# Kernel tuning notes

Measured on AMD Instinct MI355X. Metric: run time of the kernel, lower is better.

## Reference

```python
import jax, jax.numpy as jnp
import numpy as np

B, S, D, H, T = 64, 512, 1024, 1024, 9


def setup_inputs() -> dict:
    key = jax.random.key(0)
    ks = jax.random.split(key, 8)
    return {
        "input_": jax.random.normal(ks[0], (B, S, D), dtype=jnp.float32),
        "labels": jax.random.randint(ks[1], (B, S), 0, T),
        "attention_mask": jnp.ones((B, S), dtype=jnp.int32),
        # linear_1: input_dim -> hidden_dim (stored [in, out])
        "W1": (jax.random.normal(ks[2], (D, H), dtype=jnp.float32) * 0.02),
        "b1": jnp.zeros((H,), dtype=jnp.float32),
        # linear_2: hidden_dim -> tag_dim
        "W2": (jax.random.normal(ks[3], (H, T), dtype=jnp.float32) * 0.02),
        "b2": jnp.zeros((T,), dtype=jnp.float32),
        # torchcrf params: uniform(-0.1, 0.1)
        "start_trans": jax.random.uniform(ks[4], (T,), minval=-0.1, maxval=0.1),
        "end_trans": jax.random.uniform(ks[5], (T,), minval=-0.1, maxval=0.1),
        "trans": jax.random.uniform(ks[6], (T, T), minval=-0.1, maxval=0.1),
    }


def _crf_mean_llh(logits, tags, mask, start, end, trans):
    """torchcrf.CRF log-likelihood, reduction='mean'. logits [B,S,T]."""
    nb = logits.shape[0]
    em = jnp.transpose(logits, (1, 0, 2))          # [S,B,T] time-major
    tg = tags.T                                    # [S,B]
    m = mask.T.astype(logits.dtype)                # [S,B]
    bidx = jnp.arange(nb)

    # --- numerator: score of the gold path ---
    score0 = start[tg[0]] + em[0, bidx, tg[0]]

    def num_step(carry, x):
        score, last = carry
        em_t, tag_t, m_t = x
        score = score + (trans[last, tag_t] + em_t[bidx, tag_t]) * m_t
        last = jnp.where(m_t > 0, tag_t, last)
        return (score, last), None

    (score, last), _ = jax.lax.scan(num_step, (score0, tg[0]), (em[1:], tg[1:], m[1:]))
    score = score + end[last]

    # --- denominator: log-partition via logsumexp forward recurrence ---
    alpha0 = start[None, :] + em[0]                # [B,T]

    def part_step(alpha, x):
        em_t, m_t = x
        # [B, prev T, next T] semiring (log-sum-exp) matrix product
        nxt = jax.nn.logsumexp(alpha[:, :, None] + trans[None, :, :] + em_t[:, None, :], axis=1)
        alpha = jnp.where(m_t[:, None] > 0, nxt, alpha)
        return alpha, None

    alpha, _ = jax.lax.scan(part_step, alpha0, (em[1:], m[1:]))
    log_z = jax.nn.logsumexp(alpha + end[None, :], axis=1)

    return jnp.mean(score - log_z)


def reference(input_, labels, attention_mask, W1, b1, W2, b2, start_trans, end_trans, trans):
    # dropout layers are identity in eval mode
    h = input_ @ W1 + b1                           # [B,S,H]
    logits = h @ W2 + b2                           # [B,S,T]
    llh = _crf_mean_llh(logits, labels, attention_mask, start_trans, end_trans, trans)
    loss = -llh                                    # forward returns (-1*crf_llh, logits)
    return (loss, logits)
```

## Files before the change

kernel.cpp:

```cpp
#include <hip/hip_runtime.h>

#define BD 64
#define SD 512
#define DD 1024
#define HD 1024
#define TD 9
#define NSEG 16
#define SEGL 32
#define NEGI -1e30f

__device__ __forceinline__ float lse9(const float v[9]) {
    float m0 = fmaxf(v[0], v[1]);
    float m1 = fmaxf(v[2], v[3]);
    float m2 = fmaxf(v[4], v[5]);
    float m3 = fmaxf(v[6], v[7]);
    float mx = fmaxf(fmaxf(m0, m1), fmaxf(fmaxf(m2, m3), v[8]));
    float s = __expf(v[0] - mx) + __expf(v[1] - mx) + __expf(v[2] - mx)
            + __expf(v[3] - mx) + __expf(v[4] - mx) + __expf(v[5] - mx)
            + __expf(v[6] - mx) + __expf(v[7] - mx) + __expf(v[8] - mx);
    return mx + __logf(s);
}

__global__ __launch_bounds__(256) void k_w12(const float* __restrict__ W1,
                                             const float* __restrict__ b1,
                                             const float* __restrict__ W2,
                                             const float* __restrict__ b2,
                                             float* __restrict__ W12t,
                                             float* __restrict__ W12d,
                                             float* __restrict__ b12,
                                             float* __restrict__ out) {
    __shared__ float wred[4][TD];
    const int tid = threadIdx.x;
    const int wave = tid >> 6, lane = tid & 63;
    const int d = blockIdx.x;

    if (d == 0 && tid == 0) out[0] = 0.f;

    const float* row = (d < DD) ? (W1 + (size_t)d * HD) : b1;
    float4 x = ((const float4*)row)[tid];

    float w[36];
    const float4* wp = (const float4*)(W2 + (size_t)tid * 36);
#pragma unroll
    for (int u = 0; u < 9; u++) ((float4*)w)[u] = wp[u];

    float acc[TD];
#pragma unroll
    for (int t = 0; t < TD; t++)
        acc[t] = x.x * w[t] + x.y * w[9 + t] + x.z * w[18 + t] + x.w * w[27 + t];

#pragma unroll
    for (int t = 0; t < TD; t++) {
        float v = acc[t];
#pragma unroll
        for (int m = 1; m < 64; m <<= 1) v += __shfl_xor(v, m);
        acc[t] = v;
    }
    if (lane == 0) {
#pragma unroll
        for (int t = 0; t < TD; t++) wred[wave][t] = acc[t];
    }
    __syncthreads();
    if (tid < TD) {
        float s = wred[0][tid] + wred[1][tid] + wred[2][tid] + wred[3][tid];
        if (d < DD) {
            W12t[tid * DD + d] = s;
            W12d[d * TD + tid] = s;
        } else {
            b12[tid] = s + b2[tid];
        }
    }
}

__global__ __launch_bounds__(256) void k_gemm_seg(const float* __restrict__ X,
                                                  const float* __restrict__ W12t,
                                                  const float* __restrict__ b12,
                                                  const int* __restrict__ maskp,
                                                  const float* __restrict__ transp,
                                                  float* __restrict__ logits,
                                                  float* __restrict__ segP) {
    __shared__ float bufA[16 * 81];
    __shared__ float bufB[8 * 81];
    __shared__ float em[SEGL * TD];
    __shared__ int   mk[SEGL];
    __shared__ float tr[81];
    __shared__ float bb[TD];

    const int blk = blockIdx.x;
    const int b = blk >> 4, s = blk & 15;
    const int tid = threadIdx.x;
    const int wave = tid >> 6, lane = tid & 63;
    const int g = lane >> 4, l16 = lane & 15;
    const int grp = wave * 4 + g;
    const int t0 = s * SEGL;

    if (tid < TD) bb[tid] = b12[tid];
    if (tid < 81) tr[tid] = transp[tid];
    if (tid < SEGL) {
        int t = t0 + 1 + tid;
        mk[tid] = (t < SD) ? maskp[b * SD + t] : 0;
    }

    const int rowa = t0 + 1 + grp * 2;
    const int rowb_real = rowa + 1;
    const int rowb = (rowb_real < SD) ? rowb_real : (SD - 1);

    const float4* xr0 = (const float4*)(X + ((size_t)b * SD + rowa) * DD);
    const float4* xr1 = (const float4*)(X + ((size_t)b * SD + rowb) * DD);

    const float4* wr[TD];
#pragma unroll
    for (int t = 0; t < TD; t++)
        wr[t] = (const float4*)(W12t + (size_t)t * DD) + l16;

    float acc0[TD], acc1[TD];
#pragma unroll
    for (int t = 0; t < TD; t++) { acc0[t] = 0.f; acc1[t] = 0.f; }

#pragma unroll 4
    for (int k = 0; k < 16; k++) {
        float4 x0 = xr0[l16 + k * 16];
        float4 x1 = xr1[l16 + k * 16];
#pragma unroll
        for (int t = 0; t < TD; t++) {
            const float4 w = wr[t][k * 16];
            acc0[t] += x0.x * w.x + x0.y * w.y + x0.z * w.z + x0.w * w.w;
            acc1[t] += x1.x * w.x + x1.y * w.y + x1.z * w.z + x1.w * w.w;
        }
    }

#pragma unroll
    for (int t = 0; t < TD; t++) {
        float v0 = acc0[t], v1 = acc1[t];
        v0 += __shfl_xor(v0, 1); v1 += __shfl_xor(v1, 1);
        v0 += __shfl_xor(v0, 2); v1 += __shfl_xor(v1, 2);
        v0 += __shfl_xor(v0, 4); v1 += __shfl_xor(v1, 4);
        v0 += __shfl_xor(v0, 8); v1 += __shfl_xor(v1, 8);
        acc0[t] = v0; acc1[t] = v1;
    }

    if (l16 < TD) {
        float v0 = acc0[l16] + bb[l16];
        float v1 = acc1[l16] + bb[l16];
        em[(grp * 2) * TD + l16] = v0;
        em[(grp * 2 + 1) * TD + l16] = v1;
        float* o = logits + ((size_t)b * SD + rowa) * TD;
        o[l16] = v0;
        if (rowb_real < SD) o[TD + l16] = v1;
    }
    __syncthreads();

    for (int e = tid; e < 16 * 81; e += 256) {
        int p = e / 81, r = e - p * 81;
        int i = r / 9, j = r - i * 9;
        int la = 2 * p, lb = 2 * p + 1;
        int mA = mk[la], mB = mk[lb];
        float o;
        if (mA && mB) {
            float v[9];
#pragma unroll
            for (int k = 0; k < 9; k++)
                v[k] = tr[i * 9 + k] + em[la * 9 + k] + tr[k * 9 + j];
            o = lse9(v) + em[lb * 9 + j];
        } else if (mA) {
            o = tr[r] + em[la * 9 + j];
        } else if (mB) {
            o = tr[r] + em[lb * 9 + j];
        } else {
            o = (i == j) ? 0.f : NEGI;
        }
        bufA[e] = o;
    }
    __syncthreads();

#define COMBINE(SRC, DST, NP)                                        \
    for (int e = tid; e < (NP) * 81; e += 256) {                     \
        int p = e / 81, r = e - p * 81;                              \
        int i = r / 9, j = r - i * 9;                                \
        const float* Am = (SRC) + (2 * p) * 81;                      \
        const float* Bm = Am + 81;                                   \
        float v[9];                                                  \
        _Pragma("unroll")                                            \
        for (int k = 0; k < 9; k++) v[k] = Am[i * 9 + k] + Bm[k * 9 + j]; \
        (DST)[e] = lse9(v);                                          \
    }                                                                \
    __syncthreads();

    COMBINE(bufA, bufB, 8)
    COMBINE(bufB, bufA, 4)
    COMBINE(bufA, bufB, 2)

    if (tid < 81) {
        int i = tid / 9, j = tid - (tid / 9) * 9;
        float v[9];
#pragma unroll
        for (int k = 0; k < 9; k++) v[k] = bufB[i * 9 + k] + bufB[81 + k * 9 + j];
        segP[(size_t)blk * 81 + tid] = lse9(v);
    }
}

__global__ __launch_bounds__(256) void k_crf_fin(const float* __restrict__ X,
                                                 const float* __restrict__ W12d,
                                                 const float* __restrict__ b12,
                                                 const float* __restrict__ logits,
                                                 const int* __restrict__ labels,
                                                 const int* __restrict__ maskp,
                                                 const float* __restrict__ startp,
                                                 const float* __restrict__ endp,
                                                 const float* __restrict__ transp,
                                                 const float* __restrict__ segP,
                                                 float* __restrict__ logits_out0,
                                                 float* __restrict__ out) {
    const int b = blockIdx.x;
    const int tid = threadIdx.x;
    const int wave = tid >> 6, lane = tid & 63;

    __shared__ float S[16 * 81];
    __shared__ float A8[8 * 81];
    __shared__ float A4[4 * 81];
    __shared__ float A2[2 * 81];
    __shared__ float P[81];
    __shared__ float finv[81];
    __shared__ float red[256];
    __shared__ int   redi[256];
    __shared__ float wred[4][TD];
    __shared__ float row0[TD];

    {
        float4 x = ((const float4*)(X + (size_t)b * SD * DD))[tid];
        float w[36];
        const float4* wp = (const float4*)(W12d + (size_t)tid * 36);
#pragma unroll
        for (int u = 0; u < 9; u++) ((float4*)w)[u] = wp[u];
        float acc[TD];
#pragma unroll
        for (int t = 0; t < TD; t++)
            acc[t] = x.x * w[t] + x.y * w[9 + t] + x.z * w[18 + t] + x.w * w[27 + t];
#pragma unroll
        for (int t = 0; t < TD; t++) {
            float v = acc[t];
#pragma unroll
            for (int m = 1; m < 64; m <<= 1) v += __shfl_xor(v, m);
            acc[t] = v;
        }
        if (lane == 0) {
#pragma unroll
            for (int t = 0; t < TD; t++) wred[wave][t] = acc[t];
        }
    }

    for (int i = tid; i < 16 * 81; i += 256) S[i] = segP[(size_t)b * NSEG * 81 + i];
    __syncthreads();

    if (tid < TD) {
        float v = wred[0][tid] + wred[1][tid] + wred[2][tid] + wred[3][tid] + b12[tid];
        row0[tid] = v;
        logits_out0[(size_t)b * SD * TD + tid] = v;
    }

    COMBINE(S, A8, 8)
    COMBINE(A8, A4, 4)
    COMBINE(A4, A2, 2)

    if (tid < 81) {
        int i = tid / 9, j = tid - (tid / 9) * 9;
        float v[9];
#pragma unroll
        for (int k = 0; k < 9; k++) v[k] = A2[i * 9 + k] + A2[81 + k * 9 + j];
        P[tid] = lse9(v);
    }
    __syncthreads();

    if (tid < 81) {
        int k = tid / 9, j = tid - (tid / 9) * 9;
        finv[tid] = startp[k] + row0[k] + P[tid] + endp[j];
    }

    float part = 0.f;
    for (int t = 1 + tid; t < SD; t += 256) {
        if (maskp[b * SD + t]) {
            int tgp = labels[b * SD + t - 1];
            int tgc = labels[b * SD + t];
            part += transp[tgp * TD + tgc] + logits[((size_t)b * SD + t) * TD + tgc];
        }
    }
    int lastt = 0;
    for (int t = tid; t < SD; t += 256) {
        if (maskp[b * SD + t]) lastt = max(lastt, t);
    }
    red[tid] = part;
    redi[tid] = lastt;
    __syncthreads();

    if (tid < 64) {
        float p4 = red[tid] + red[tid + 64] + red[tid + 128] + red[tid + 192];
        int l4 = max(max(redi[tid], redi[tid + 64]), max(redi[tid + 128], redi[tid + 192]));
#pragma unroll
        for (int m = 1; m < 64; m <<= 1) {
            p4 += __shfl_xor(p4, m);
            l4 = max(l4, __shfl_xor(l4, m));
        }
        float v1 = finv[tid];
        float v2 = (tid + 64 < 81) ? finv[tid + 64] : NEGI;
        float mx = fmaxf(v1, v2);
#pragma unroll
        for (int m = 1; m < 64; m <<= 1) mx = fmaxf(mx, __shfl_xor(mx, m));
        float ssum = __expf(v1 - mx) + __expf(v2 - mx);
#pragma unroll
        for (int m = 1; m < 64; m <<= 1) ssum += __shfl_xor(ssum, m);
        float logz = mx + __logf(ssum);

        if (tid == 0) {
            int tg0 = labels[b * SD];
            int tgl = labels[b * SD + l4];
            float score = p4 + startp[tg0] + row0[tg0] + endp[tgl];
            atomicAdd(out, -(score - logz) / (float)BD);
        }
    }
}

extern "C" void kernel_launch(void* const* d_in, const int* in_sizes, int n_in,
                              void* d_out, int out_size, void* d_ws, size_t ws_size,
                              hipStream_t stream) {
    const float* X      = (const float*)d_in[0];
    const int*   labels = (const int*)d_in[1];
    const int*   maskp  = (const int*)d_in[2];
    const float* W1     = (const float*)d_in[3];
    const float* b1     = (const float*)d_in[4];
    const float* W2     = (const float*)d_in[5];
    const float* b2     = (const float*)d_in[6];
    const float* startp = (const float*)d_in[7];
    const float* endp   = (const float*)d_in[8];
    const float* transp = (const float*)d_in[9];

    float* out = (float*)d_out;
    float* ws = (float*)d_ws;

    float* W12t = ws + 64;
    float* b12  = ws + 64 + DD * TD;
    float* segP = ws + 64 + DD * TD + 16;
    float* W12d = segP + (size_t)BD * NSEG * 81;
    float* logits = out + 1;

    hipLaunchKernelGGL(k_w12, dim3(DD + 1), dim3(256), 0, stream,
                       W1, b1, W2, b2, W12t, W12d, b12, out);
    hipLaunchKernelGGL(k_gemm_seg, dim3(BD * NSEG), dim3(256), 0, stream,
                       X, W12t, b12, maskp, transp, logits, segP);
    hipLaunchKernelGGL(k_crf_fin, dim3(BD), dim3(256), 0, stream,
                       X, W12d, b12, logits, labels, maskp, startp, endp, transp,
                       segP, logits, out);
}
```

Before: 66.97 us.

## Split sequence into 32 segments of 16 rows to double block count

Halves the segment length so the fused GEMV+CRF-segment kernel launches twice as many blocks (2048), with each 16-lane group computing one row instead of two. The finishing kernel gains an extra log-semiring combine level to reduce 32 segment matrices per batch. The aim is more parallelism and latency hiding on the bandwidth-bound X read, at the cost of redundant W12 reads per block, more segP traffic, and a longer serial reduction in the final kernel.

```diff
diff --git a/kernel.cpp b/kernel.cpp
--- a/kernel.cpp
+++ b/kernel.cpp
@@ -5,8 +5,8 @@
 #define DD 1024
 #define HD 1024
 #define TD 9
-#define NSEG 16
-#define SEGL 32
+#define NSEG 32
+#define SEGL 16
 #define NEGI -1e30f
 
 __device__ __forceinline__ float lse9(const float v[9]) {
@@ -79,15 +79,15 @@
                                                   const float* __restrict__ transp,
                                                   float* __restrict__ logits,
                                                   float* __restrict__ segP) {
-    __shared__ float bufA[16 * 81];
-    __shared__ float bufB[8 * 81];
+    __shared__ float bufA[8 * 81];
+    __shared__ float bufB[4 * 81];
     __shared__ float em[SEGL * TD];
     __shared__ int   mk[SEGL];
     __shared__ float tr[81];
     __shared__ float bb[TD];
 
     const int blk = blockIdx.x;
-    const int b = blk >> 4, s = blk & 15;
+    const int b = blk >> 5, s = blk & 31;
     const int tid = threadIdx.x;
     const int wave = tid >> 6, lane = tid & 63;
     const int g = lane >> 4, l16 = lane & 15;
@@ -100,57 +100,52 @@
         int t = t0 + 1 + tid;
         mk[tid] = (t < SD) ? maskp[b * SD + t] : 0;
     }
-
-    const int rowa = t0 + 1 + grp * 2;
-    const int rowb_real = rowa + 1;
-    const int rowb = (rowb_real < SD) ? rowb_real : (SD - 1);
-
-    const float4* xr0 = (const float4*)(X + ((size_t)b * SD + rowa) * DD);
-    const float4* xr1 = (const float4*)(X + ((size_t)b * SD + rowb) * DD);
+    __syncthreads();
+
+    const int rowa = t0 + 1 + grp;
+    const int rowc = (rowa < SD) ? rowa : (SD - 1);
+    const float4* xr = (const float4*)(X + ((size_t)b * SD + rowc) * DD);
 
     const float4* wr[TD];
 #pragma unroll
     for (int t = 0; t < TD; t++)
         wr[t] = (const float4*)(W12t + (size_t)t * DD) + l16;
 
-    float acc0[TD], acc1[TD];
-#pragma unroll
-    for (int t = 0; t < TD; t++) { acc0[t] = 0.f; acc1[t] = 0.f; }
+    float acc[TD];
+#pragma unroll
+    for (int t = 0; t < TD; t++) acc[t] = 0.f;
 
 #pragma unroll 4
     for (int k = 0; k < 16; k++) {
-        float4 x0 = xr0[l16 + k * 16];
-        float4 x1 = xr1[l16 + k * 16];
+        float4 x0 = xr[l16 + k * 16];
 #pragma unroll
         for (int t = 0; t < TD; t++) {
             const float4 w = wr[t][k * 16];
-            acc0[t] += x0.x * w.x + x0.y * w.y + x0.z * w.z + x0.w * w.w;
-            acc1[t] += x1.x * w.x + x1.y * w.y + x1.z * w.z + x1.w * w.w;
+            acc[t] += x0.x * w.x + x0.y * w.y + x0.z * w.z + x0.w * w.w;
         }
     }
 
 #pragma unroll
     for (int t = 0; t < TD; t++) {
-        float v0 = acc0[t], v1 = acc1[t];
-        v0 += __shfl_xor(v0, 1); v1 += __shfl_xor(v1, 1);
-        v0 += __shfl_xor(v0, 2); v1 += __shfl_xor(v1, 2);
-        v0 += __shfl_xor(v0, 4); v1 += __shfl_xor(v1, 4);
-        v0 += __shfl_xor(v0, 8); v1 += __shfl_xor(v1, 8);
-        acc0[t] = v0; acc1[t] = v1;
+        float v = acc[t];
+        v += __shfl_xor(v, 1);
+        v += __shfl_xor(v, 2);
+        v += __shfl_xor(v, 4);
+        v += __shfl_xor(v, 8);
+        acc[t] = v;
     }
 
     if (l16 < TD) {
-        float v0 = acc0[l16] + bb[l16];
-        float v1 = acc1[l16] + bb[l16];
-        em[(grp * 2) * TD + l16] = v0;
-        em[(grp * 2 + 1) * TD + l16] = v1;
-        float* o = logits + ((size_t)b * SD + rowa) * TD;
-        o[l16] = v0;
-        if (rowb_real < SD) o[TD + l16] = v1;
-    }
-    __syncthreads();
-
-    for (int e = tid; e < 16 * 81; e += 256) {
+        float v0 = acc[l16] + bb[l16];
+        em[grp * TD + l16] = v0;
+        if (rowa < SD) {
+            float* o = logits + ((size_t)b * SD + rowa) * TD;
+            o[l16] = v0;
+        }
+    }
+    __syncthreads();
+
+    for (int e = tid; e < 8 * 81; e += 256) {
         int p = e / 81, r = e - p * 81;
         int i = r / 9, j = r - i * 9;
         int la = 2 * p, lb = 2 * p + 1;
@@ -186,15 +181,14 @@
     }                                                                \
     __syncthreads();
 
-    COMBINE(bufA, bufB, 8)
-    COMBINE(bufB, bufA, 4)
-    COMBINE(bufA, bufB, 2)
+    COMBINE(bufA, bufB, 4)
+    COMBINE(bufB, bufA, 2)
 
     if (tid < 81) {
         int i = tid / 9, j = tid - (tid / 9) * 9;
         float v[9];
 #pragma unroll
-        for (int k = 0; k < 9; k++) v[k] = bufB[i * 9 + k] + bufB[81 + k * 9 + j];
+        for (int k = 0; k < 9; k++) v[k] = bufA[i * 9 + k] + bufA[81 + k * 9 + j];
         segP[(size_t)blk * 81 + tid] = lse9(v);
     }
 }
@@ -215,7 +209,8 @@
     const int tid = threadIdx.x;
     const int wave = tid >> 6, lane = tid & 63;
 
-    __shared__ float S[16 * 81];
+    __shared__ float S[32 * 81];
+    __shared__ float A16[16 * 81];
     __shared__ float A8[8 * 81];
     __shared__ float A4[4 * 81];
     __shared__ float A2[2 * 81];
@@ -249,7 +244,7 @@
         }
     }
 
-    for (int i = tid; i < 16 * 81; i += 256) S[i] = segP[(size_t)b * NSEG * 81 + i];
+    for (int i = tid; i < 32 * 81; i += 256) S[i] = segP[(size_t)b * NSEG * 81 + i];
     __syncthreads();
 
     if (tid < TD) {
@@ -258,7 +253,8 @@
         logits_out0[(size_t)b * SD * TD + tid] = v;
     }
 
-    COMBINE(S, A8, 8)
+    COMBINE(S, A16, 16)
+    COMBINE(A16, A8, 8)
     COMBINE(A8, A4, 4)
     COMBINE(A4, A2, 2)
 
```

Result: slower. 93.80 us (+40.1%).
